# Kernel tuning notes

Hardware: AMD Instinct MI355X
Metric: run time of the kernel (lower is better)

## Reference

```python
import jax, jax.numpy as jnp
import numpy as np

B, L, H, NH, P = 4, 1024, 1024, 16, 2048
HD = H // NH


def setup_inputs() -> dict:
    key = jax.random.key(0)
    ks = jax.random.split(key, 6)
    x = jax.random.normal(ks[0], (B, L, H), dtype=jnp.float32)
    # torch.nn.Linear weights are [out, in]
    Wqkv = jax.random.normal(ks[1], (3 * H, H), dtype=jnp.float32) * 0.02
    bqkv = jnp.zeros((3 * H,), dtype=jnp.float32)
    Wo = jax.random.normal(ks[2], (H, H), dtype=jnp.float32) * 0.02
    bo = jnp.zeros((H,), dtype=jnp.float32)
    Er = jax.random.normal(ks[3], (NH, P, HD), dtype=jnp.float32)
    # causal mask: True where attention is disallowed (masked_fill semantics)
    mask = jnp.triu(jnp.ones((L, L), dtype=bool), k=1)
    return {"x": x, "mask": mask, "Wqkv": Wqkv, "bqkv": bqkv,
            "Wo": Wo, "bo": bo, "Er": Er}


def reference(x, mask, Wqkv, bqkv, Wo, bo, Er):
    b, l, d = x.shape
    nh, p, hd = Er.shape
    qkv = x @ Wqkv.T + bqkv                      # [b, l, 3d]
    q, k, v = jnp.split(qkv, 3, axis=-1)
    q = q.reshape(b, l, nh, hd).transpose(0, 2, 1, 3)   # [b, nh, l, hd]
    k = k.reshape(b, l, nh, hd).transpose(0, 2, 1, 3)
    v = v.reshape(b, l, nh, hd).transpose(0, 2, 1, 3)

    scores = jnp.einsum('bnlh,bnkh->bnlk', q, k) / jnp.sqrt(
        jnp.asarray(hd, dtype=x.dtype))

    # relative positions (j - i), torch negative-index wraparound -> mod p
    pos = jnp.arange(l)
    rel = (pos[None, :] - pos[:, None]) % p      # [l, l] in [0, p)
    # Equivalent to einsum('bnlh,rnlkh->bnlk', q, Er[:, rel][None]) but
    # computed as q @ Er^T over all positions then gathered (same math,
    # avoids materializing the [nh, l, l, hd] tensor).
    QEr_full = jnp.einsum('bnlh,nph->bnlp', q, Er)       # [b, nh, l, p]
    i_idx = pos[:, None]                          # broadcasts with rel
    QEr = QEr_full[:, :, i_idx, rel]              # [b, nh, l, l]

    a = scores + QEr
    a = jnp.where(mask, -jnp.inf, a)
    a = jax.nn.softmax(a, axis=-1)                # dropout: eval mode (identity)

    out = jnp.einsum('bnlk,bnkh->bnlh', a, v)     # [b, nh, l, hd]
    out = out.transpose(0, 2, 1, 3).reshape(b, l, d)
    return out @ Wo.T + bo
```

## Files before the change

### kernel.cpp

```cpp
#include <hip/hip_runtime.h>

typedef unsigned short u16;
typedef __bf16 bf16x8 __attribute__((ext_vector_type(8)));
typedef unsigned short u16x8 __attribute__((ext_vector_type(8)));
typedef unsigned short u16x4 __attribute__((ext_vector_type(4)));
typedef float f32x4 __attribute__((ext_vector_type(4)));

#define MFMA16(a, b, c) __builtin_amdgcn_mfma_f32_16x16x32_bf16((a), (b), (c), 0, 0, 0)

#define WAVE_LDS_FENCE() do { \
  asm volatile("s_waitcnt lgkmcnt(0)" ::: "memory"); \
  __builtin_amdgcn_sched_barrier(0); \
} while (0)

#define RAW_BARRIER() do { \
  __builtin_amdgcn_sched_barrier(0); \
  __builtin_amdgcn_s_barrier(); \
  __builtin_amdgcn_sched_barrier(0); \
} while (0)

#define TOP_BARRIER() do { \
  asm volatile("s_waitcnt lgkmcnt(0)" ::: "memory"); \
  RAW_BARRIER(); \
} while (0)

#define PIPE_WAIT(N) do { \
  asm volatile("s_waitcnt vmcnt(" #N ")" ::: "memory"); \
  __builtin_amdgcn_sched_barrier(0); \
  __builtin_amdgcn_s_barrier(); \
  __builtin_amdgcn_sched_barrier(0); \
} while (0)

#define GLDS(gp, lp) __builtin_amdgcn_global_load_lds( \
    (const __attribute__((address_space(1))) unsigned int*)(gp), \
    (__attribute__((address_space(3))) unsigned int*)(lp), 16, 0, 0)

__device__ __forceinline__ u16 f2b(float f) {
  unsigned u = __float_as_uint(f);
  u += 0x7fffu + ((u >> 16) & 1u);
  return (u16)(u >> 16);
}
__device__ __forceinline__ float b2f(u16 h) {
  return __uint_as_float(((unsigned)h) << 16);
}

__global__ void cvt_all(const float* __restrict__ x, u16* __restrict__ xb,
                        const float* __restrict__ w1, u16* __restrict__ w1b,
                        const float* __restrict__ w2, u16* __restrict__ w2b) {
  int i = blockIdx.x * blockDim.x + threadIdx.x;
  const float* s; u16* d; int off;
  if (i < 1048576)      { s = x;  d = xb;  off = i; }
  else if (i < 1835008) { s = w1; d = w1b; off = i - 1048576; }
  else                  { s = w2; d = w2b; off = i - 1835008; }
  float4 v = *(const float4*)(s + (size_t)off * 4);
  *(ushort4*)(d + (size_t)off * 4) = make_ushort4(f2b(v.x), f2b(v.y), f2b(v.z), f2b(v.w));
}

__global__ void build_F(const float* __restrict__ Er, u16* __restrict__ Fb) {
  int i = blockIdx.x * blockDim.x + threadIdx.x;
  int base = i * 4;
  int d = base & 63;
  int m = (base >> 6) & 1023;
  int n = base >> 16;
  int sm = (2048 - m) & 2047;
  float4 v = *(const float4*)(Er + ((size_t)(n * 2048 + sm) * 64 + d));
  *(ushort4*)(Fb + (size_t)base) = make_ushort4(f2b(v.x), f2b(v.y), f2b(v.z), f2b(v.w));
}

__global__ __launch_bounds__(256) void gemm_qkv(const u16* __restrict__ A, const u16* __restrict__ Bw,
                                                const float* __restrict__ bias,
                                                u16* __restrict__ Qo, u16* __restrict__ Ko,
                                                u16* __restrict__ Vt) {
  __shared__ u16 As[3][4][128][8];
  __shared__ u16 Bs[3][4][128][8];
  const int orig = blockIdx.y * 24 + blockIdx.x;
  const int xcd = orig & 7, q = orig >> 3;
  const int mt = ((xcd >> 1) << 3) + q / 12;
  const int nt = (xcd & 1) * 12 + q % 12;
  const int m0 = mt * 128, n0 = nt * 128;
  const int t = threadIdx.x, lane = t & 63, w = t >> 6;
  const int wr = w >> 1, wc = w & 1;
  const int l16 = lane & 15, lg = lane >> 4;
  f32x4 acc[4][4] = {};
  const int r0 = t & 127, g0 = t >> 7;
  const int g1 = g0 + 2;

#define STAGE(buf, k0) do { \
    GLDS(&A[(size_t)(m0 + r0) * 1024 + (k0) + g0 * 8], &As[buf][g0][r0][0]); \
    GLDS(&A[(size_t)(m0 + r0) * 1024 + (k0) + g1 * 8], &As[buf][g1][r0][0]); \
    GLDS(&Bw[(size_t)(n0 + r0) * 1024 + (k0) + g0 * 8], &Bs[buf][g0][r0][0]); \
    GLDS(&Bw[(size_t)(n0 + r0) * 1024 + (k0) + g1 * 8], &Bs[buf][g1][r0][0]); \
  } while (0)

  STAGE(0, 0);
  STAGE(1, 32);

  int buf = 0;
  for (int kt = 0; kt < 32; ++kt) {
    if (kt < 31) PIPE_WAIT(4); else PIPE_WAIT(0);
    if (kt < 30) {
      int nb = buf + 2; if (nb >= 3) nb -= 3;
      STAGE(nb, (kt + 2) * 32);
      __builtin_amdgcn_sched_barrier(0);
    }
    bf16x8 af[4], bfr[4];
#pragma unroll
    for (int m = 0; m < 4; ++m) af[m] = *(const bf16x8*)&As[buf][lg][wr * 64 + m * 16 + l16][0];
#pragma unroll
    for (int n = 0; n < 4; ++n) bfr[n] = *(const bf16x8*)&Bs[buf][lg][wc * 64 + n * 16 + l16][0];
#pragma unroll
    for (int m = 0; m < 4; ++m)
#pragma unroll
      for (int n = 0; n < 4; ++n) acc[m][n] = MFMA16(af[m], bfr[n], acc[m][n]);
    if (++buf == 3) buf = 0;
  }
#undef STAGE

#pragma unroll
  for (int n = 0; n < 4; ++n) {
    int col = n0 + wc * 64 + n * 16 + l16;
    float bq = bias[col];
    int which = col >> 10;
    int h = col & 1023;
    int head = h >> 6, d = h & 63;
    if (which == 2) {
#pragma unroll
      for (int m = 0; m < 4; ++m) {
        int row = m0 + wr * 64 + m * 16 + lg * 4;
        int b = row >> 10, ii = row & 1023;
        u16x4 o;
#pragma unroll
        for (int r = 0; r < 4; ++r) o[r] = f2b(acc[m][n][r] + bq);
        *(u16x4*)&Vt[(size_t)(((b * 16 + head) << 6) + d) * 1024 + ii] = o;
      }
    } else {
      u16* dst = which == 0 ? Qo : Ko;
      float scale = which == 1 ? 0.125f : 1.0f;
#pragma unroll
      for (int m = 0; m < 4; ++m) {
#pragma unroll
        for (int r = 0; r < 4; ++r) {
          int row = m0 + wr * 64 + m * 16 + lg * 4 + r;
          int b = row >> 10, ii = row & 1023;
          dst[(size_t)(((b * 16 + head) << 10) + ii) * 64 + d] = f2b((acc[m][n][r] + bq) * scale);
        }
      }
    }
  }
}

__global__ __launch_bounds__(256) void gemm_out(const u16* __restrict__ A, const u16* __restrict__ Bw,
                                                const float* __restrict__ bias, float* __restrict__ Co) {
  __shared__ u16 As[3][4][128][8];
  __shared__ u16 Bs[3][4][128][8];
  const int orig = blockIdx.y * 8 + blockIdx.x;
  const int xcd = orig & 7, q = orig >> 3;
  const int mt = (xcd << 2) + (q >> 3);
  const int nt = q & 7;
  const int m0 = mt * 128, n0 = nt * 128;
  const int t = threadIdx.x, lane = t & 63, w = t >> 6;
  const int wr = w >> 1, wc = w & 1;
  const int l16 = lane & 15, lg = lane >> 4;
  f32x4 acc[4][4] = {};
  const int r0 = t & 127, g0 = t >> 7;
  const int g1 = g0 + 2;

#define STAGE(buf, k0) do { \
    GLDS(&A[(size_t)(m0 + r0) * 1024 + (k0) + g0 * 8], &As[buf][g0][r0][0]); \
    GLDS(&A[(size_t)(m0 + r0) * 1024 + (k0) + g1 * 8], &As[buf][g1][r0][0]); \
    GLDS(&Bw[(size_t)(n0 + r0) * 1024 + (k0) + g0 * 8], &Bs[buf][g0][r0][0]); \
    GLDS(&Bw[(size_t)(n0 + r0) * 1024 + (k0) + g1 * 8], &Bs[buf][g1][r0][0]); \
  } while (0)

  STAGE(0, 0);
  STAGE(1, 32);

  int buf = 0;
  for (int kt = 0; kt < 32; ++kt) {
    if (kt < 31) PIPE_WAIT(4); else PIPE_WAIT(0);
    if (kt < 30) {
      int nb = buf + 2; if (nb >= 3) nb -= 3;
      STAGE(nb, (kt + 2) * 32);
      __builtin_amdgcn_sched_barrier(0);
    }
    bf16x8 af[4], bfr[4];
#pragma unroll
    for (int m = 0; m < 4; ++m) af[m] = *(const bf16x8*)&As[buf][lg][wr * 64 + m * 16 + l16][0];
#pragma unroll
    for (int n = 0; n < 4; ++n) bfr[n] = *(const bf16x8*)&Bs[buf][lg][wc * 64 + n * 16 + l16][0];
#pragma unroll
    for (int m = 0; m < 4; ++m)
#pragma unroll
      for (int n = 0; n < 4; ++n) acc[m][n] = MFMA16(af[m], bfr[n], acc[m][n]);
    if (++buf == 3) buf = 0;
  }
#undef STAGE

#pragma unroll
  for (int n = 0; n < 4; ++n) {
    int col = n0 + wc * 64 + n * 16 + l16;
    float bq = bias[col];
#pragma unroll
    for (int m = 0; m < 4; ++m) {
#pragma unroll
      for (int r = 0; r < 4; ++r) {
        int row = m0 + wr * 64 + m * 16 + lg * 4 + r;
        Co[(size_t)row * 1024 + col] = acc[m][n][r] + bq;
      }
    }
  }
}

__global__ __launch_bounds__(256) void attn_kernel(const u16* __restrict__ Qg, const u16* __restrict__ Kg,
                                                   const u16* __restrict__ Vtg, const u16* __restrict__ Fg,
                                                   u16* __restrict__ AO) {
  __shared__ u16 Kl[4096];
  __shared__ u16 Vl[4096];
  __shared__ u16 Fl[8192];
  __shared__ u16 BP[4][1024];

  const int bn = blockIdx.x;
  const int b = bn >> 4, n = bn & 15;
  const int qt = 15 - (int)blockIdx.y;
  const int i0 = qt * 64;
  const int t = threadIdx.x, lane = t & 63, w = t >> 6;
  const int l16 = lane & 15, lg = lane >> 4;

  const int rr0 = t >> 3, cc0 = t & 7;
  const int rr1 = (t + 256) >> 3, cc1 = t & 7;

  bf16x8 qf[2];
  {
    const u16* qp = &Qg[(size_t)((bn << 10) + i0 + (w << 4) + l16) * 64 + lg * 8];
    qf[0] = *(const bf16x8*)qp;
    qf[1] = *(const bf16x8*)(qp + 32);
  }

  {
    int mb0 = i0 - 63;
    int h0 = 64 + rr0, h1 = 64 + rr1;
    int gm0 = mb0 + h0; gm0 = gm0 < 0 ? 0 : (gm0 > 1023 ? 1023 : gm0);
    int gm1 = mb0 + h1; gm1 = gm1 < 0 ? 0 : (gm1 > 1023 ? 1023 : gm1);
    u16x8 a = *(const u16x8*)&Fg[(size_t)((n << 10) + gm0) * 64 + cc0 * 8];
    u16x8 c = *(const u16x8*)&Fg[(size_t)((n << 10) + gm1) * 64 + cc1 * 8];
    *(u16x8*)&Fl[h0 * 64 + (((cc0 ^ (h0 & 7)) & 7) << 3)] = a;
    *(u16x8*)&Fl[h1 * 64 + (((cc1 ^ (h1 & 7)) & 7) << 3)] = c;
  }

  float mrun[4], lsum[4];
  f32x4 ao[4] = {};
#pragma unroll
  for (int r = 0; r < 4; ++r) { mrun[r] = -3.0e38f; lsum[r] = 0.0f; }

  u16x8 rk0, rk1, rv0, rv1, rf0, rf1;

#define LOAD_STAGE(jt_) do { \
    int j0_ = (jt_) * 64, mb_ = i0 - j0_ - 63; \
    rk0 = *(const u16x8*)&Kg[(size_t)((bn << 10) + j0_ + rr0) * 64 + cc0 * 8]; \
    rk1 = *(const u16x8*)&Kg[(size_t)((bn << 10) + j0_ + rr1) * 64 + cc1 * 8]; \
    rv0 = *(const u16x8*)&Vtg[(size_t)((bn << 6) + rr0) * 1024 + j0_ + cc0 * 8]; \
    rv1 = *(const u16x8*)&Vtg[(size_t)((bn << 6) + rr1) * 1024 + j0_ + cc1 * 8]; \
    int m0_ = mb_ + rr0; m0_ = m0_ < 0 ? 0 : (m0_ > 1023 ? 1023 : m0_); \
    int m1_ = mb_ + rr1; m1_ = m1_ < 0 ? 0 : (m1_ > 1023 ? 1023 : m1_); \
    rf0 = *(const u16x8*)&Fg[(size_t)((n << 10) + m0_) * 64 + cc0 * 8]; \
    rf1 = *(const u16x8*)&Fg[(size_t)((n << 10) + m1_) * 64 + cc1 * 8]; \
  } while (0)

  LOAD_STAGE(0);

  for (int jt = 0; jt <= qt; ++jt) {
    const bool diag = (jt == qt);
    const int ph = (jt & 1) << 6;

    *(u16x8*)&Kl[rr0 * 64 + (((cc0 ^ (rr0 & 7)) & 7) << 3)] = rk0;
    *(u16x8*)&Kl[rr1 * 64 + (((cc1 ^ (rr1 & 7)) & 7) << 3)] = rk1;
    *(u16x8*)&Vl[rr0 * 64 + (((cc0 ^ (rr0 & 7)) & 7) << 3)] = rv0;
    *(u16x8*)&Vl[rr1 * 64 + (((cc1 ^ (rr1 & 7)) & 7) << 3)] = rv1;
    *(u16x8*)&Fl[(rr0 ^ ph) * 64 + (((cc0 ^ (rr0 & 7)) & 7) << 3)] = rf0;
    *(u16x8*)&Fl[(rr1 ^ ph) * 64 + (((cc1 ^ (rr1 & 7)) & 7) << 3)] = rf1;
    TOP_BARRIER();

    if (jt < qt) LOAD_STAGE(jt + 1);

    __builtin_amdgcn_s_setprio(1);
    f32x4 sc[4] = {};
#pragma unroll
    for (int kk = 0; kk < 2; ++kk)
#pragma unroll
      for (int nn = 0; nn < 4; ++nn) {
        int jr = nn * 16 + l16;
        bf16x8 kb = *(const bf16x8*)&Kl[jr * 64 + ((((lg + 4 * kk) ^ (jr & 7)) & 7) << 3)];
        sc[nn] = MFMA16(qf[kk], kb, sc[nn]);
      }
    f32x4 bb[5] = {};
#pragma unroll
    for (int kk = 0; kk < 2; ++kk)
#pragma unroll
      for (int ct = 0; ct < 5; ++ct) {
        int trow = (w << 4) + ct * 16 + l16;
        bf16x8 fb = *(const bf16x8*)&Fl[(trow ^ ph) * 64 + ((((lg + 4 * kk) ^ (trow & 7)) & 7) << 3)];
        bb[ct] = MFMA16(qf[kk], fb, bb[ct]);
      }
    __builtin_amdgcn_s_setprio(0);

#pragma unroll
    for (int ct = 0; ct < 5; ++ct)
#pragma unroll
      for (int r = 0; r < 4; ++r) {
        int il = lg * 4 + r;
        int jl = il + 63 - (ct * 16 + l16);
        if ((unsigned)jl < 64u)
          BP[w][il * 64 + ((jl & 15) << 2) + (jl >> 4)] = f2b(bb[ct][r]);
      }
    WAVE_LDS_FENCE();

    float pv[4][4];
    float lmax[4];
#pragma unroll
    for (int r = 0; r < 4; ++r) {
      int il = lg * 4 + r;
      u16x4 gv = *(const u16x4*)&BP[w][il * 64 + (l16 << 2)];
      float m4 = -3.0e38f;
#pragma unroll
      for (int nn = 0; nn < 4; ++nn) {
        int jl = nn * 16 + l16;
        float s = sc[nn][r] + b2f(gv[nn]);
        if (diag && jl > (w << 4) + il) s = -1.0e30f;
        pv[nn][r] = s;
        m4 = fmaxf(m4, s);
      }
      lmax[r] = m4;
    }
    bool ok = (lmax[0] <= mrun[0] + 8.0f) && (lmax[1] <= mrun[1] + 8.0f) &&
              (lmax[2] <= mrun[2] + 8.0f) && (lmax[3] <= mrun[3] + 8.0f);
    if (__all(ok)) {
#pragma unroll
      for (int r = 0; r < 4; ++r) {
        float rs = 0.0f;
#pragma unroll
        for (int nn = 0; nn < 4; ++nn) {
          pv[nn][r] = __expf(pv[nn][r] - mrun[r]);
          rs += pv[nn][r];
        }
        lsum[r] += rs;
      }
    } else {
#pragma unroll
      for (int r = 0; r < 4; ++r) {
        float mx = lmax[r];
#pragma unroll
        for (int off = 1; off < 16; off <<= 1) mx = fmaxf(mx, __shfl_xor(mx, off));
        float mnew = fmaxf(mrun[r], mx);
        float scl = __expf(mrun[r] - mnew);
        float rs = 0.0f;
#pragma unroll
        for (int nn = 0; nn < 4; ++nn) {
          pv[nn][r] = __expf(pv[nn][r] - mnew);
          rs += pv[nn][r];
        }
        lsum[r] = lsum[r] * scl + rs;
        mrun[r] = mnew;
#pragma unroll
        for (int nd = 0; nd < 4; ++nd) ao[nd][r] *= scl;
      }
    }

#pragma unroll
    for (int nn = 0; nn < 4; ++nn)
#pragma unroll
      for (int r = 0; r < 4; ++r) {
        int i = lg * 4 + r, j = nn * 16 + l16;
        BP[w][i * 64 + ((((j >> 3) ^ (i & 7)) & 7) << 3) + (j & 7)] = f2b(pv[nn][r]);
      }
    WAVE_LDS_FENCE();
    __builtin_amdgcn_s_setprio(1);
#pragma unroll
    for (int kk = 0; kk < 2; ++kk) {
      bf16x8 pa = *(const bf16x8*)&BP[w][l16 * 64 + ((((lg + 4 * kk) ^ (l16 & 7)) & 7) << 3)];
#pragma unroll
      for (int nd = 0; nd < 4; ++nd) {
        int dr = nd * 16 + l16;
        bf16x8 vb = *(const bf16x8*)&Vl[dr * 64 + ((((lg + 4 * kk) ^ (dr & 7)) & 7) << 3)];
        ao[nd] = MFMA16(pa, vb, ao[nd]);
      }
    }
    __builtin_amdgcn_s_setprio(0);
    RAW_BARRIER();
  }

#pragma unroll
  for (int r = 0; r < 4; ++r)
#pragma unroll
    for (int off = 1; off < 16; off <<= 1) lsum[r] += __shfl_xor(lsum[r], off);

#pragma unroll
  for (int nd = 0; nd < 4; ++nd)
#pragma unroll
    for (int r = 0; r < 4; ++r) {
      int i = i0 + (w << 4) + lg * 4 + r;
      int d = nd * 16 + l16;
      float v = ao[nd][r] / lsum[r];
      AO[(size_t)((b << 10) + i) * 1024 + n * 64 + d] = f2b(v);
    }
#undef LOAD_STAGE
}

extern "C" void kernel_launch(void* const* d_in, const int* in_sizes, int n_in,
                              void* d_out, int out_size, void* d_ws, size_t ws_size,
                              hipStream_t stream) {
  (void)in_sizes; (void)n_in; (void)out_size; (void)ws_size;
  const float* x    = (const float*)d_in[0];
  const float* Wqkv = (const float*)d_in[2];
  const float* bqkv = (const float*)d_in[3];
  const float* Wo   = (const float*)d_in[4];
  const float* bo   = (const float*)d_in[5];
  const float* Er   = (const float*)d_in[6];
  float* out = (float*)d_out;

  char* p = (char*)d_ws;
  u16* xb    = (u16*)p; p += (size_t)4096 * 1024 * 2;
  u16* wqkvb = (u16*)p; p += (size_t)3072 * 1024 * 2;
  u16* wob   = (u16*)p; p += (size_t)1024 * 1024 * 2;
  u16* Fb    = (u16*)p; p += (size_t)16 * 1024 * 64 * 2;
  u16* Qb    = (u16*)p; p += (size_t)64 * 1024 * 64 * 2;
  u16* Kb    = (u16*)p; p += (size_t)64 * 1024 * 64 * 2;
  u16* Vtb   = (u16*)p; p += (size_t)64 * 1024 * 64 * 2;
  u16* AO    = (u16*)p; p += (size_t)4096 * 1024 * 2;

  cvt_all<<<8192, 256, 0, stream>>>(x, xb, Wqkv, wqkvb, Wo, wob);
  build_F<<<1024, 256, 0, stream>>>(Er, Fb);
  gemm_qkv<<<dim3(24, 32), 256, 0, stream>>>(xb, wqkvb, bqkv, Qb, Kb, Vtb);
  attn_kernel<<<dim3(64, 16), 256, 0, stream>>>(Qb, Kb, Vtb, Fb, AO);
  gemm_out<<<dim3(8, 32), 256, 0, stream>>>(AO, wob, bo, out);
}
```

Measured before the change: 148.5 us.

## Enlarge attention query tile to 128 rows with two sub-rows per wave

Each attention block now processes 128 query rows instead of 64, so each wave handles two 16-row subtiles that share every K/V LDS load and its MFMA B-operand reads. The relative-position F tile moves to a three-slot ring buffer in LDS, and the per-tile causal mask is computed from global indices on every iteration. Query tiles are dispatched in an interleaved long/short order to balance causal work across blocks. The grid is halved to 512 blocks, and register and LDS use per block go up, which may reduce occupancy and leave fewer blocks to fill the GPU.

Measured after the change: 189.3 us. 27.4% more time.

```diff
diff --git a/kernel.cpp b/kernel.cpp
--- a/kernel.cpp
+++ b/kernel.cpp
@@ -216,172 +216,203 @@
                                                    u16* __restrict__ AO) {
   __shared__ u16 Kl[4096];
   __shared__ u16 Vl[4096];
-  __shared__ u16 Fl[8192];
-  __shared__ u16 BP[4][1024];
+  __shared__ u16 Fl[12288];
+  __shared__ u16 BP[4][2048];
 
   const int bn = blockIdx.x;
   const int b = bn >> 4, n = bn & 15;
-  const int qt = 15 - (int)blockIdx.y;
-  const int i0 = qt * 64;
+  const int QTLUT[8] = {7, 0, 6, 1, 5, 2, 4, 3};
+  const int qt = QTLUT[blockIdx.y];
+  const int i0 = qt * 128;
+  const int nt = 2 * qt + 2;
   const int t = threadIdx.x, lane = t & 63, w = t >> 6;
   const int l16 = lane & 15, lg = lane >> 4;
 
   const int rr0 = t >> 3, cc0 = t & 7;
   const int rr1 = (t + 256) >> 3, cc1 = t & 7;
 
-  bf16x8 qf[2];
-  {
-    const u16* qp = &Qg[(size_t)((bn << 10) + i0 + (w << 4) + l16) * 64 + lg * 8];
-    qf[0] = *(const bf16x8*)qp;
-    qf[1] = *(const bf16x8*)(qp + 32);
-  }
-
-  {
-    int mb0 = i0 - 63;
-    int h0 = 64 + rr0, h1 = 64 + rr1;
-    int gm0 = mb0 + h0; gm0 = gm0 < 0 ? 0 : (gm0 > 1023 ? 1023 : gm0);
-    int gm1 = mb0 + h1; gm1 = gm1 < 0 ? 0 : (gm1 > 1023 ? 1023 : gm1);
-    u16x8 a = *(const u16x8*)&Fg[(size_t)((n << 10) + gm0) * 64 + cc0 * 8];
-    u16x8 c = *(const u16x8*)&Fg[(size_t)((n << 10) + gm1) * 64 + cc1 * 8];
-    *(u16x8*)&Fl[h0 * 64 + (((cc0 ^ (h0 & 7)) & 7) << 3)] = a;
-    *(u16x8*)&Fl[h1 * 64 + (((cc1 ^ (h1 & 7)) & 7) << 3)] = c;
-  }
-
-  float mrun[4], lsum[4];
-  f32x4 ao[4] = {};
-#pragma unroll
-  for (int r = 0; r < 4; ++r) { mrun[r] = -3.0e38f; lsum[r] = 0.0f; }
+  bf16x8 qf[2][2];
+#pragma unroll
+  for (int sr = 0; sr < 2; ++sr) {
+    const u16* qp = &Qg[(size_t)((bn << 10) + i0 + 32 * w + 16 * sr + l16) * 64 + lg * 8];
+    qf[sr][0] = *(const bf16x8*)qp;
+    qf[sr][1] = *(const bf16x8*)(qp + 32);
+  }
+
+#pragma unroll
+  for (int s = 0; s < 6; ++s) {
+    int ch = t + 256 * s;
+    int prow = ch >> 3, c = ch & 7;
+    int m = i0 - 63 + prow;
+    m = m < 0 ? 0 : (m > 1023 ? 1023 : m);
+    u16x8 v = *(const u16x8*)&Fg[(size_t)((n << 10) + m) * 64 + c * 8];
+    *(u16x8*)&Fl[prow * 64 + (((c ^ (prow & 7)) & 7) << 3)] = v;
+  }
+
+  float mrun[2][4], lsum[2][4];
+  f32x4 ao[2][4] = {};
+#pragma unroll
+  for (int sr = 0; sr < 2; ++sr)
+#pragma unroll
+    for (int r = 0; r < 4; ++r) { mrun[sr][r] = -3.0e38f; lsum[sr][r] = 0.0f; }
 
   u16x8 rk0, rk1, rv0, rv1, rf0, rf1;
 
-#define LOAD_STAGE(jt_) do { \
-    int j0_ = (jt_) * 64, mb_ = i0 - j0_ - 63; \
+#define LOAD_KV(jt_) do { \
+    int j0_ = (jt_) * 64; \
     rk0 = *(const u16x8*)&Kg[(size_t)((bn << 10) + j0_ + rr0) * 64 + cc0 * 8]; \
     rk1 = *(const u16x8*)&Kg[(size_t)((bn << 10) + j0_ + rr1) * 64 + cc1 * 8]; \
     rv0 = *(const u16x8*)&Vtg[(size_t)((bn << 6) + rr0) * 1024 + j0_ + cc0 * 8]; \
     rv1 = *(const u16x8*)&Vtg[(size_t)((bn << 6) + rr1) * 1024 + j0_ + cc1 * 8]; \
+  } while (0)
+
+#define LOAD_F(jt_) do { \
+    int mb_ = i0 - 64 * (jt_) - 63; \
     int m0_ = mb_ + rr0; m0_ = m0_ < 0 ? 0 : (m0_ > 1023 ? 1023 : m0_); \
     int m1_ = mb_ + rr1; m1_ = m1_ < 0 ? 0 : (m1_ > 1023 ? 1023 : m1_); \
     rf0 = *(const u16x8*)&Fg[(size_t)((n << 10) + m0_) * 64 + cc0 * 8]; \
     rf1 = *(const u16x8*)&Fg[(size_t)((n << 10) + m1_) * 64 + cc1 * 8]; \
   } while (0)
 
-  LOAD_STAGE(0);
-
-  for (int jt = 0; jt <= qt; ++jt) {
-    const bool diag = (jt == qt);
-    const int ph = (jt & 1) << 6;
+  LOAD_KV(0);
+
+  for (int jt = 0; jt < nt; ++jt) {
+    const int j0 = jt * 64;
 
     *(u16x8*)&Kl[rr0 * 64 + (((cc0 ^ (rr0 & 7)) & 7) << 3)] = rk0;
     *(u16x8*)&Kl[rr1 * 64 + (((cc1 ^ (rr1 & 7)) & 7) << 3)] = rk1;
     *(u16x8*)&Vl[rr0 * 64 + (((cc0 ^ (rr0 & 7)) & 7) << 3)] = rv0;
     *(u16x8*)&Vl[rr1 * 64 + (((cc1 ^ (rr1 & 7)) & 7) << 3)] = rv1;
-    *(u16x8*)&Fl[(rr0 ^ ph) * 64 + (((cc0 ^ (rr0 & 7)) & 7) << 3)] = rf0;
-    *(u16x8*)&Fl[(rr1 ^ ph) * 64 + (((cc1 ^ (rr1 & 7)) & 7) << 3)] = rf1;
+    if (jt >= 1) {
+      int fb = 64 * ((3 - (jt % 3)) % 3);
+      *(u16x8*)&Fl[(fb + rr0) * 64 + (((cc0 ^ (rr0 & 7)) & 7) << 3)] = rf0;
+      *(u16x8*)&Fl[(fb + rr1) * 64 + (((cc1 ^ (rr1 & 7)) & 7) << 3)] = rf1;
+    }
     TOP_BARRIER();
 
-    if (jt < qt) LOAD_STAGE(jt + 1);
+    if (jt + 1 < nt) { LOAD_KV(jt + 1); LOAD_F(jt + 1); }
 
     __builtin_amdgcn_s_setprio(1);
-    f32x4 sc[4] = {};
+    f32x4 sc[2][4] = {};
 #pragma unroll
     for (int kk = 0; kk < 2; ++kk)
 #pragma unroll
       for (int nn = 0; nn < 4; ++nn) {
         int jr = nn * 16 + l16;
         bf16x8 kb = *(const bf16x8*)&Kl[jr * 64 + ((((lg + 4 * kk) ^ (jr & 7)) & 7) << 3)];
-        sc[nn] = MFMA16(qf[kk], kb, sc[nn]);
-      }
-    f32x4 bb[5] = {};
-#pragma unroll
-    for (int kk = 0; kk < 2; ++kk)
-#pragma unroll
-      for (int ct = 0; ct < 5; ++ct) {
-        int trow = (w << 4) + ct * 16 + l16;
-        bf16x8 fb = *(const bf16x8*)&Fl[(trow ^ ph) * 64 + ((((lg + 4 * kk) ^ (trow & 7)) & 7) << 3)];
-        bb[ct] = MFMA16(qf[kk], fb, bb[ct]);
+        sc[0][nn] = MFMA16(qf[0][kk], kb, sc[0][nn]);
+        sc[1][nn] = MFMA16(qf[1][kk], kb, sc[1][nn]);
       }
     __builtin_amdgcn_s_setprio(0);
 
 #pragma unroll
-    for (int ct = 0; ct < 5; ++ct)
+    for (int sr = 0; sr < 2; ++sr) {
+      __builtin_amdgcn_s_setprio(1);
+      f32x4 bb[5] = {};
+#pragma unroll
+      for (int kk = 0; kk < 2; ++kk)
+#pragma unroll
+        for (int ct = 0; ct < 5; ++ct) {
+          int base_s = (32 * w + 16 * sr + 16 * ct + 1536 - 64 * jt) % 192;
+          int prow = base_s + l16;
+          bf16x8 fb = *(const bf16x8*)&Fl[prow * 64 + ((((lg + 4 * kk) ^ (prow & 7)) & 7) << 3)];
+          bb[ct] = MFMA16(qf[sr][kk], fb, bb[ct]);
+        }
+      __builtin_amdgcn_s_setprio(0);
+#pragma unroll
+      for (int ct = 0; ct < 5; ++ct)
+#pragma unroll
+        for (int r = 0; r < 4; ++r) {
+          int ils = lg * 4 + r;
+          int jl = ils + 63 - (ct * 16 + l16);
+          if ((unsigned)jl < 64u)
+            BP[w][(sr * 16 + ils) * 64 + ((jl & 15) << 2) + (jl >> 4)] = f2b(bb[ct][r]);
+        }
+    }
+    WAVE_LDS_FENCE();
+
+    float pv[2][4][4];
+    float lmax[2][4];
+#pragma unroll
+    for (int sr = 0; sr < 2; ++sr)
 #pragma unroll
       for (int r = 0; r < 4; ++r) {
-        int il = lg * 4 + r;
-        int jl = il + 63 - (ct * 16 + l16);
-        if ((unsigned)jl < 64u)
-          BP[w][il * 64 + ((jl & 15) << 2) + (jl >> 4)] = f2b(bb[ct][r]);
-      }
-    WAVE_LDS_FENCE();
-
-    float pv[4][4];
-    float lmax[4];
-#pragma unroll
-    for (int r = 0; r < 4; ++r) {
-      int il = lg * 4 + r;
-      u16x4 gv = *(const u16x4*)&BP[w][il * 64 + (l16 << 2)];
-      float m4 = -3.0e38f;
-#pragma unroll
-      for (int nn = 0; nn < 4; ++nn) {
-        int jl = nn * 16 + l16;
-        float s = sc[nn][r] + b2f(gv[nn]);
-        if (diag && jl > (w << 4) + il) s = -1.0e30f;
-        pv[nn][r] = s;
-        m4 = fmaxf(m4, s);
-      }
-      lmax[r] = m4;
-    }
-    bool ok = (lmax[0] <= mrun[0] + 8.0f) && (lmax[1] <= mrun[1] + 8.0f) &&
-              (lmax[2] <= mrun[2] + 8.0f) && (lmax[3] <= mrun[3] + 8.0f);
+        int il = sr * 16 + lg * 4 + r;
+        int ig = i0 + 32 * w + 16 * sr + lg * 4 + r;
+        u16x4 gv = *(const u16x4*)&BP[w][il * 64 + (l16 << 2)];
+        float m4 = -3.0e38f;
+#pragma unroll
+        for (int nn = 0; nn < 4; ++nn) {
+          int jg = j0 + nn * 16 + l16;
+          float s = sc[sr][nn][r] + b2f(gv[nn]);
+          if (jg > ig) s = -1.0e30f;
+          pv[sr][nn][r] = s;
+          m4 = fmaxf(m4, s);
+        }
+        lmax[sr][r] = m4;
+      }
+    bool ok = true;
+#pragma unroll
+    for (int sr = 0; sr < 2; ++sr)
+#pragma unroll
+      for (int r = 0; r < 4; ++r) ok = ok && (lmax[sr][r] <= mrun[sr][r] + 8.0f);
     if (__all(ok)) {
 #pragma unroll
-      for (int r = 0; r < 4; ++r) {
-        float rs = 0.0f;
-#pragma unroll
-        for (int nn = 0; nn < 4; ++nn) {
-          pv[nn][r] = __expf(pv[nn][r] - mrun[r]);
-          rs += pv[nn][r];
-        }
-        lsum[r] += rs;
-      }
+      for (int sr = 0; sr < 2; ++sr)
+#pragma unroll
+        for (int r = 0; r < 4; ++r) {
+          float rs = 0.0f;
+#pragma unroll
+          for (int nn = 0; nn < 4; ++nn) {
+            pv[sr][nn][r] = __expf(pv[sr][nn][r] - mrun[sr][r]);
+            rs += pv[sr][nn][r];
+          }
+          lsum[sr][r] += rs;
+        }
     } else {
 #pragma unroll
-      for (int r = 0; r < 4; ++r) {
-        float mx = lmax[r];
-#pragma unroll
-        for (int off = 1; off < 16; off <<= 1) mx = fmaxf(mx, __shfl_xor(mx, off));
-        float mnew = fmaxf(mrun[r], mx);
-        float scl = __expf(mrun[r] - mnew);
-        float rs = 0.0f;
-#pragma unroll
-        for (int nn = 0; nn < 4; ++nn) {
-          pv[nn][r] = __expf(pv[nn][r] - mnew);
-          rs += pv[nn][r];
-        }
-        lsum[r] = lsum[r] * scl + rs;
-        mrun[r] = mnew;
-#pragma unroll
-        for (int nd = 0; nd < 4; ++nd) ao[nd][r] *= scl;
-      }
-    }
-
-#pragma unroll
-    for (int nn = 0; nn < 4; ++nn)
-#pragma unroll
-      for (int r = 0; r < 4; ++r) {
-        int i = lg * 4 + r, j = nn * 16 + l16;
-        BP[w][i * 64 + ((((j >> 3) ^ (i & 7)) & 7) << 3) + (j & 7)] = f2b(pv[nn][r]);
-      }
+      for (int sr = 0; sr < 2; ++sr)
+#pragma unroll
+        for (int r = 0; r < 4; ++r) {
+          float mx = lmax[sr][r];
+#pragma unroll
+          for (int off = 1; off < 16; off <<= 1) mx = fmaxf(mx, __shfl_xor(mx, off));
+          float mnew = fmaxf(mrun[sr][r], mx);
+          float scl = __expf(mrun[sr][r] - mnew);
+          float rs = 0.0f;
+#pragma unroll
+          for (int nn = 0; nn < 4; ++nn) {
+            pv[sr][nn][r] = __expf(pv[sr][nn][r] - mnew);
+            rs += pv[sr][nn][r];
+          }
+          lsum[sr][r] = lsum[sr][r] * scl + rs;
+          mrun[sr][r] = mnew;
+#pragma unroll
+          for (int nd = 0; nd < 4; ++nd) ao[sr][nd][r] *= scl;
+        }
+    }
+
+#pragma unroll
+    for (int sr = 0; sr < 2; ++sr)
+#pragma unroll
+      for (int nn = 0; nn < 4; ++nn)
+#pragma unroll
+        for (int r = 0; r < 4; ++r) {
+          int i = sr * 16 + lg * 4 + r, j = nn * 16 + l16;
+          BP[w][i * 64 + ((((j >> 3) ^ (i & 7)) & 7) << 3) + (j & 7)] = f2b(pv[sr][nn][r]);
+        }
     WAVE_LDS_FENCE();
     __builtin_amdgcn_s_setprio(1);
 #pragma unroll
     for (int kk = 0; kk < 2; ++kk) {
-      bf16x8 pa = *(const bf16x8*)&BP[w][l16 * 64 + ((((lg + 4 * kk) ^ (l16 & 7)) & 7) << 3)];
+      bf16x8 pa0 = *(const bf16x8*)&BP[w][l16 * 64 + ((((lg + 4 * kk) ^ (l16 & 7)) & 7) << 3)];
+      bf16x8 pa1 = *(const bf16x8*)&BP[w][(16 + l16) * 64 + ((((lg + 4 * kk) ^ (l16 & 7)) & 7) << 3)];
 #pragma unroll
       for (int nd = 0; nd < 4; ++nd) {
         int dr = nd * 16 + l16;
         bf16x8 vb = *(const bf16x8*)&Vl[dr * 64 + ((((lg + 4 * kk) ^ (dr & 7)) & 7) << 3)];
-        ao[nd] = MFMA16(pa, vb, ao[nd]);
+        ao[0][nd] = MFMA16(pa0, vb, ao[0][nd]);
+        ao[1][nd] = MFMA16(pa1, vb, ao[1][nd]);
       }
     }
     __builtin_amdgcn_s_setprio(0);
@@ -389,20 +420,25 @@
   }
 
 #pragma unroll
-  for (int r = 0; r < 4; ++r)
-#pragma unroll
-    for (int off = 1; off < 16; off <<= 1) lsum[r] += __shfl_xor(lsum[r], off);
-
-#pragma unroll
-  for (int nd = 0; nd < 4; ++nd)
-#pragma unroll
-    for (int r = 0; r < 4; ++r) {
-      int i = i0 + (w << 4) + lg * 4 + r;
-      int d = nd * 16 + l16;
-      float v = ao[nd][r] / lsum[r];
-      AO[(size_t)((b << 10) + i) * 1024 + n * 64 + d] = f2b(v);
-    }
-#undef LOAD_STAGE
+  for (int sr = 0; sr < 2; ++sr)
+#pragma unroll
+    for (int r = 0; r < 4; ++r)
+#pragma unroll
+      for (int off = 1; off < 16; off <<= 1) lsum[sr][r] += __shfl_xor(lsum[sr][r], off);
+
+#pragma unroll
+  for (int sr = 0; sr < 2; ++sr)
+#pragma unroll
+    for (int nd = 0; nd < 4; ++nd)
+#pragma unroll
+      for (int r = 0; r < 4; ++r) {
+        int i = i0 + 32 * w + 16 * sr + lg * 4 + r;
+        int d = nd * 16 + l16;
+        float v = ao[sr][nd][r] / lsum[sr][r];
+        AO[(size_t)((b << 10) + i) * 1024 + n * 64 + d] = f2b(v);
+      }
+#undef LOAD_KV
+#undef LOAD_F
 }
 
 extern "C" void kernel_launch(void* const* d_in, const int* in_sizes, int n_in,
@@ -430,6 +466,6 @@
   cvt_all<<<8192, 256, 0, stream>>>(x, xb, Wqkv, wqkvb, Wo, wob);
   build_F<<<1024, 256, 0, stream>>>(Er, Fb);
   gemm_qkv<<<dim3(24, 32), 256, 0, stream>>>(xb, wqkvb, bqkv, Qb, Kb, Vtb);
-  attn_kernel<<<dim3(64, 16), 256, 0, stream>>>(Qb, Kb, Vtb, Fb, AO);
+  attn_kernel<<<dim3(64, 8), 256, 0, stream>>>(Qb, Kb, Vtb, Fb, AO);
   gemm_out<<<dim3(8, 32), 256, 0, stream>>>(AO, wob, bo, out);
 }
```
